# Kernel optimization log

Hardware: AMD Instinct MI355X
Metric: run time of the kernel (lower is better)

## Reference

```python
import jax, jax.numpy as jnp
import numpy as np

B, C, K = 128, 32, 128


def setup_inputs() -> dict:
    key = jax.random.key(0)
    k1, k2, k3, k4, k5 = jax.random.split(key, 5)
    x = jax.random.normal(k1, (B, 1, K, K), dtype=jnp.float32)
    # Conv2d(1, C, (1, K)) weight -> effectively [C, K] over the column axis
    w_col = jax.random.normal(k2, (C, K), dtype=jnp.float32) * (1.0 / np.sqrt(K))
    b_col = jax.random.normal(k3, (C,), dtype=jnp.float32) * 0.01
    # Conv2d(1, C, (K, 1)) weight -> effectively [C, K] over the row axis
    w_row = jax.random.normal(k4, (C, K), dtype=jnp.float32) * (1.0 / np.sqrt(K))
    b_row = jax.random.normal(k5, (C,), dtype=jnp.float32) * 0.01
    return {"x": x, "w_col": w_col, "b_col": b_col, "w_row": w_row, "b_row": b_row}


def reference(x, w_col, b_col, w_row, b_row):
    xs = x[:, 0]  # [B, K, K]
    # conv_column: kernel (1, K) contracts the column axis j -> [B, C, K] (rows i)
    col = jnp.einsum("bij,cj->bci", xs, w_col) + b_col[None, :, None]
    # conv_row: kernel (K, 1) contracts the row axis i -> [B, C, K] (cols j)
    row = jnp.einsum("bij,ci->bcj", xs, w_row) + b_row[None, :, None]
    # Tiling conv_row to [B,C,K,K] (identical rows) and conv_column to
    # [B,C,K,K] (identical columns) and matmul-ing yields, for every (i, j):
    #   out[b,c,i,j] = sum_k row[b,c,k] * col[b,c,k]
    # i.e. a per-(b,c) scalar broadcast over the K x K plane.
    s = jnp.einsum("bck,bck->bc", row, col)  # [B, C]
    return jnp.broadcast_to(s[:, :, None, None], (x.shape[0], w_col.shape[0], K, K))
```

## Files before the change

### kernel.cpp

```cpp
#include <hip/hip_runtime.h>
#include <hip/hip_bf16.h>


constexpr int KDIM = 128;
constexpr int CDIM = 32;
constexpr int LD   = 132;

__device__ __forceinline__ int swz_word(int row, int col) {
    return (row << 7) | ((((col >> 2) ^ ((row >> 2) & 7)) << 2) | (col & 3));
}

__global__ __launch_bounds__(512) void fused_kernel(
    const float* __restrict__ x,
    const float* __restrict__ w_col, const float* __restrict__ b_col,
    const float* __restrict__ w_row, const float* __restrict__ b_row,
    float* __restrict__ out)
{
    __shared__ float  xs[KDIM * LD];
    __shared__ float  xt[KDIM * KDIM];
    __shared__ float2 wpr[KDIM][8];
    __shared__ float2 wpc[KDIM][8];
    __shared__ float  s_lds[16];

    const int bid = blockIdx.x;
    const int xcd = bid & 7;
    const int idx = bid >> 3;
    const int b   = xcd * 16 + (idx >> 1);
    const int ch  = idx & 1;
    const int C0  = ch * 16;
    const int tid = threadIdx.x;

    #pragma unroll
    for (int e = 0; e < 2; ++e) {
        const int ent = tid + 512 * e;
        const int i   = ent & 127;
        const int g   = ent >> 7;
        wpr[i][g] = make_float2(w_row[(C0 + g) * KDIM + i],
                                w_row[(C0 + g + 8) * KDIM + i]);
        wpc[i][g] = make_float2(w_col[(C0 + g) * KDIM + i],
                                w_col[(C0 + g + 8) * KDIM + i]);
    }

    const float4* xsrc = reinterpret_cast<const float4*>(x + (size_t)b * KDIM * KDIM);
    const int tj  = tid & 31;
    const int ti0 = tid >> 5;
    #pragma unroll
    for (int it = 0; it < 2; ++it) {
        const int ti = ti0 + 16 * it;
        const float4 r0 = xsrc[(4 * ti + 0) * 32 + tj];
        const float4 r1 = xsrc[(4 * ti + 1) * 32 + tj];
        const float4 r2 = xsrc[(4 * ti + 2) * 32 + tj];
        const float4 r3 = xsrc[(4 * ti + 3) * 32 + tj];
        *reinterpret_cast<float4*>(&xs[(4 * ti + 0) * LD + 4 * tj]) = r0;
        *reinterpret_cast<float4*>(&xs[(4 * ti + 1) * LD + 4 * tj]) = r1;
        *reinterpret_cast<float4*>(&xs[(4 * ti + 2) * LD + 4 * tj]) = r2;
        *reinterpret_cast<float4*>(&xs[(4 * ti + 3) * LD + 4 * tj]) = r3;
        *reinterpret_cast<float4*>(&xt[swz_word(4 * tj + 0, 4 * ti)]) =
            make_float4(r0.x, r1.x, r2.x, r3.x);
        *reinterpret_cast<float4*>(&xt[swz_word(4 * tj + 1, 4 * ti)]) =
            make_float4(r0.y, r1.y, r2.y, r3.y);
        *reinterpret_cast<float4*>(&xt[swz_word(4 * tj + 2, 4 * ti)]) =
            make_float4(r0.z, r1.z, r2.z, r3.z);
        *reinterpret_cast<float4*>(&xt[swz_word(4 * tj + 3, 4 * ti)]) =
            make_float4(r0.w, r1.w, r2.w, r3.w);
    }
    __syncthreads();

    const int w    = tid >> 6;
    const int lane = tid & 63;
    const int kq   = lane & 31;
    const int ih   = lane >> 5;
    const int k0   = 4 * kq;

    float au0[4] = {0,0,0,0}, au1[4] = {0,0,0,0};
    float av0[4] = {0,0,0,0}, av1[4] = {0,0,0,0};

    #pragma unroll 4
    for (int ii = 0; ii < 64; ++ii) {
        const int i = ih * 64 + ii;
        const float4 xv = *reinterpret_cast<const float4*>(&xs[i * LD + k0]);
        const float4 tv = *reinterpret_cast<const float4*>(&xt[swz_word(i, k0)]);
        const float2 wu = wpr[i][w];
        const float2 wv = wpc[i][w];
        au0[0] = fmaf(wu.x, xv.x, au0[0]); au0[1] = fmaf(wu.x, xv.y, au0[1]);
        au0[2] = fmaf(wu.x, xv.z, au0[2]); au0[3] = fmaf(wu.x, xv.w, au0[3]);
        au1[0] = fmaf(wu.y, xv.x, au1[0]); au1[1] = fmaf(wu.y, xv.y, au1[1]);
        au1[2] = fmaf(wu.y, xv.z, au1[2]); au1[3] = fmaf(wu.y, xv.w, au1[3]);
        av0[0] = fmaf(wv.x, tv.x, av0[0]); av0[1] = fmaf(wv.x, tv.y, av0[1]);
        av0[2] = fmaf(wv.x, tv.z, av0[2]); av0[3] = fmaf(wv.x, tv.w, av0[3]);
        av1[0] = fmaf(wv.y, tv.x, av1[0]); av1[1] = fmaf(wv.y, tv.y, av1[1]);
        av1[2] = fmaf(wv.y, tv.z, av1[2]); av1[3] = fmaf(wv.y, tv.w, av1[3]);
    }

    #pragma unroll
    for (int q = 0; q < 4; ++q) {
        au0[q] += __shfl_xor(au0[q], 32);
        au1[q] += __shfl_xor(au1[q], 32);
        av0[q] += __shfl_xor(av0[q], 32);
        av1[q] += __shfl_xor(av1[q], 32);
    }
    const int c0 = C0 + w, c1 = C0 + w + 8;
    const float br0 = b_row[c0], bc0 = b_col[c0];
    const float br1 = b_row[c1], bc1 = b_col[c1];

    float p0 = 0.f, p1 = 0.f;
    #pragma unroll
    for (int q = 0; q < 4; ++q) {
        p0 += (au0[q] + br0) * (av0[q] + bc0);
        p1 += (au1[q] + br1) * (av1[q] + bc1);
    }
    #pragma unroll
    for (int off = 1; off < 32; off <<= 1) {
        p0 += __shfl_xor(p0, off);
        p1 += __shfl_xor(p1, off);
    }
    if (lane == 0) { s_lds[w] = p0; s_lds[w + 8] = p1; }
    __syncthreads();

    float4* out4 = reinterpret_cast<float4*>(out);
    #pragma unroll
    for (int cl = 0; cl < 16; ++cl) {
        const float val = s_lds[cl];
        float4 v4;
        v4.x = v4.y = v4.z = v4.w = val;
        float4* o = out4 + (size_t)(b * CDIM + C0 + cl) * 4096;
        #pragma unroll
        for (int r = 0; r < 8; ++r) {
            o[tid + 512 * r] = v4;
        }
    }
}

extern "C" void kernel_launch(void* const* d_in, const int* in_sizes, int n_in,
                              void* d_out, int out_size, void* d_ws, size_t ws_size,
                              hipStream_t stream) {
    const float* x     = (const float*)d_in[0];
    const float* w_col = (const float*)d_in[1];
    const float* b_col = (const float*)d_in[2];
    const float* w_row = (const float*)d_in[3];
    const float* b_row = (const float*)d_in[4];
    float* out = (float*)d_out;

    fused_kernel<<<256, 512, 0, stream>>>(x, w_col, b_col, w_row, b_row, out);
}
```

Baseline: 52.20 us.

## Pack x and its transpose as bf16 pairs in one LDS array; per-wave output stores

```diff
diff --git a/kernel.cpp b/kernel.cpp
--- a/kernel.cpp
+++ b/kernel.cpp
@@ -4,10 +4,13 @@
 
 constexpr int KDIM = 128;
 constexpr int CDIM = 32;
-constexpr int LD   = 132;
 
-__device__ __forceinline__ int swz_word(int row, int col) {
-    return (row << 7) | ((((col >> 2) ^ ((row >> 2) & 7)) << 2) | (col & 3));
+__device__ __forceinline__ uint32_t bf16rne(float f) {
+    const uint32_t u = __float_as_uint(f);
+    return (u + 0x7FFFu + ((u >> 16) & 1u)) >> 16;
+}
+__device__ __forceinline__ uint32_t pack2(float lo, float hi) {
+    return bf16rne(lo) | (bf16rne(hi) << 16);
 }
 
 __global__ __launch_bounds__(512) void fused_kernel(
@@ -16,29 +19,28 @@
     const float* __restrict__ w_row, const float* __restrict__ b_row,
     float* __restrict__ out)
 {
-    __shared__ float  xs[KDIM * LD];
-    __shared__ float  xt[KDIM * KDIM];
-    __shared__ float2 wpr[KDIM][8];
-    __shared__ float2 wpc[KDIM][8];
-    __shared__ float  s_lds[16];
+    __shared__ uint32_t xz[KDIM * KDIM];
+    __shared__ float4   wall[KDIM][8];
 
-    const int bid = blockIdx.x;
-    const int xcd = bid & 7;
-    const int idx = bid >> 3;
-    const int b   = xcd * 16 + (idx >> 1);
-    const int ch  = idx & 1;
-    const int C0  = ch * 16;
-    const int tid = threadIdx.x;
+    const int bid  = blockIdx.x;
+    const int xcd  = bid & 7;
+    const int idx  = bid >> 3;
+    const int b    = xcd * 16 + (idx >> 1);
+    const int ch   = idx & 1;
+    const int C0   = ch * 16;
+    const int tid  = threadIdx.x;
+    const int w    = tid >> 6;
+    const int lane = tid & 63;
 
     #pragma unroll
     for (int e = 0; e < 2; ++e) {
         const int ent = tid + 512 * e;
         const int i   = ent & 127;
         const int g   = ent >> 7;
-        wpr[i][g] = make_float2(w_row[(C0 + g) * KDIM + i],
-                                w_row[(C0 + g + 8) * KDIM + i]);
-        wpc[i][g] = make_float2(w_col[(C0 + g) * KDIM + i],
-                                w_col[(C0 + g + 8) * KDIM + i]);
+        wall[i][g] = make_float4(w_row[(C0 + g) * KDIM + i],
+                                 w_row[(C0 + g + 8) * KDIM + i],
+                                 w_col[(C0 + g) * KDIM + i],
+                                 w_col[(C0 + g + 8) * KDIM + i]);
     }
 
     const float4* xsrc = reinterpret_cast<const float4*>(x + (size_t)b * KDIM * KDIM);
@@ -47,49 +49,45 @@
     #pragma unroll
     for (int it = 0; it < 2; ++it) {
         const int ti = ti0 + 16 * it;
-        const float4 r0 = xsrc[(4 * ti + 0) * 32 + tj];
-        const float4 r1 = xsrc[(4 * ti + 1) * 32 + tj];
-        const float4 r2 = xsrc[(4 * ti + 2) * 32 + tj];
-        const float4 r3 = xsrc[(4 * ti + 3) * 32 + tj];
-        *reinterpret_cast<float4*>(&xs[(4 * ti + 0) * LD + 4 * tj]) = r0;
-        *reinterpret_cast<float4*>(&xs[(4 * ti + 1) * LD + 4 * tj]) = r1;
-        *reinterpret_cast<float4*>(&xs[(4 * ti + 2) * LD + 4 * tj]) = r2;
-        *reinterpret_cast<float4*>(&xs[(4 * ti + 3) * LD + 4 * tj]) = r3;
-        *reinterpret_cast<float4*>(&xt[swz_word(4 * tj + 0, 4 * ti)]) =
-            make_float4(r0.x, r1.x, r2.x, r3.x);
-        *reinterpret_cast<float4*>(&xt[swz_word(4 * tj + 1, 4 * ti)]) =
-            make_float4(r0.y, r1.y, r2.y, r3.y);
-        *reinterpret_cast<float4*>(&xt[swz_word(4 * tj + 2, 4 * ti)]) =
-            make_float4(r0.z, r1.z, r2.z, r3.z);
-        *reinterpret_cast<float4*>(&xt[swz_word(4 * tj + 3, 4 * ti)]) =
-            make_float4(r0.w, r1.w, r2.w, r3.w);
+        float4 A[4], Bq[4];
+        #pragma unroll
+        for (int r = 0; r < 4; ++r) A[r]  = xsrc[(4 * ti + r) * 32 + tj];
+        #pragma unroll
+        for (int r = 0; r < 4; ++r) Bq[r] = xsrc[(4 * tj + r) * 32 + ti];
+        #pragma unroll
+        for (int r = 0; r < 4; ++r) {
+            uint4 e;
+            e.x = pack2(A[r].x, (&Bq[0].x)[r]);
+            e.y = pack2(A[r].y, (&Bq[1].x)[r]);
+            e.z = pack2(A[r].z, (&Bq[2].x)[r]);
+            e.w = pack2(A[r].w, (&Bq[3].x)[r]);
+            *reinterpret_cast<uint4*>(&xz[(4 * ti + r) * KDIM + 4 * tj]) = e;
+        }
     }
     __syncthreads();
 
-    const int w    = tid >> 6;
-    const int lane = tid & 63;
-    const int kq   = lane & 31;
-    const int ih   = lane >> 5;
-    const int k0   = 4 * kq;
+    const int kq = lane & 31;
+    const int ih = lane >> 5;
+    const int k0 = 4 * kq;
 
     float au0[4] = {0,0,0,0}, au1[4] = {0,0,0,0};
     float av0[4] = {0,0,0,0}, av1[4] = {0,0,0,0};
 
-    #pragma unroll 4
+    #pragma unroll 8
     for (int ii = 0; ii < 64; ++ii) {
         const int i = ih * 64 + ii;
-        const float4 xv = *reinterpret_cast<const float4*>(&xs[i * LD + k0]);
-        const float4 tv = *reinterpret_cast<const float4*>(&xt[swz_word(i, k0)]);
-        const float2 wu = wpr[i][w];
-        const float2 wv = wpc[i][w];
-        au0[0] = fmaf(wu.x, xv.x, au0[0]); au0[1] = fmaf(wu.x, xv.y, au0[1]);
-        au0[2] = fmaf(wu.x, xv.z, au0[2]); au0[3] = fmaf(wu.x, xv.w, au0[3]);
-        au1[0] = fmaf(wu.y, xv.x, au1[0]); au1[1] = fmaf(wu.y, xv.y, au1[1]);
-        au1[2] = fmaf(wu.y, xv.z, au1[2]); au1[3] = fmaf(wu.y, xv.w, au1[3]);
-        av0[0] = fmaf(wv.x, tv.x, av0[0]); av0[1] = fmaf(wv.x, tv.y, av0[1]);
-        av0[2] = fmaf(wv.x, tv.z, av0[2]); av0[3] = fmaf(wv.x, tv.w, av0[3]);
-        av1[0] = fmaf(wv.y, tv.x, av1[0]); av1[1] = fmaf(wv.y, tv.y, av1[1]);
-        av1[2] = fmaf(wv.y, tv.z, av1[2]); av1[3] = fmaf(wv.y, tv.w, av1[3]);
+        const uint4  z  = *reinterpret_cast<const uint4*>(&xz[i * KDIM + k0]);
+        const float4 wq = wall[i][w];
+        const uint32_t zz[4] = {z.x, z.y, z.z, z.w};
+        #pragma unroll
+        for (int q = 0; q < 4; ++q) {
+            const float xlo = __uint_as_float(zz[q] << 16);
+            const float xhi = __uint_as_float(zz[q] & 0xFFFF0000u);
+            au0[q] = fmaf(wq.x, xlo, au0[q]);
+            au1[q] = fmaf(wq.y, xlo, au1[q]);
+            av0[q] = fmaf(wq.z, xhi, av0[q]);
+            av1[q] = fmaf(wq.w, xhi, av1[q]);
+        }
     }
 
     #pragma unroll
@@ -114,21 +112,15 @@
         p0 += __shfl_xor(p0, off);
         p1 += __shfl_xor(p1, off);
     }
-    if (lane == 0) { s_lds[w] = p0; s_lds[w + 8] = p1; }
-    __syncthreads();
 
-    float4* out4 = reinterpret_cast<float4*>(out);
+    float4 v0; v0.x = v0.y = v0.z = v0.w = p0;
+    float4 v1; v1.x = v1.y = v1.z = v1.w = p1;
+    float4* o0 = reinterpret_cast<float4*>(out) + (size_t)(b * CDIM + c0) * 4096;
+    float4* o1 = reinterpret_cast<float4*>(out) + (size_t)(b * CDIM + c1) * 4096;
     #pragma unroll
-    for (int cl = 0; cl < 16; ++cl) {
-        const float val = s_lds[cl];
-        float4 v4;
-        v4.x = v4.y = v4.z = v4.w = val;
-        float4* o = out4 + (size_t)(b * CDIM + C0 + cl) * 4096;
-        #pragma unroll
-        for (int r = 0; r < 8; ++r) {
-            o[tid + 512 * r] = v4;
-        }
-    }
+    for (int r = 0; r < 64; ++r) o0[lane + 64 * r] = v0;
+    #pragma unroll
+    for (int r = 0; r < 64; ++r) o1[lane + 64 * r] = v1;
 }
 
 extern "C" void kernel_launch(void* const* d_in, const int* in_sizes, int n_in,
```

Result: slower. 54.52 us (+4.4%).

## Split waves into row/column roles computing four channels each from LDS

Applied to the files above, without the earlier changes.

```diff
diff --git a/kernel.cpp b/kernel.cpp
--- a/kernel.cpp
+++ b/kernel.cpp
@@ -4,7 +4,6 @@
 
 constexpr int KDIM = 128;
 constexpr int CDIM = 32;
-constexpr int LD   = 132;
 
 __device__ __forceinline__ int swz_word(int row, int col) {
     return (row << 7) | ((((col >> 2) ^ ((row >> 2) & 7)) << 2) | (col & 3));
@@ -16,29 +15,32 @@
     const float* __restrict__ w_row, const float* __restrict__ b_row,
     float* __restrict__ out)
 {
-    __shared__ float  xs[KDIM * LD];
-    __shared__ float  xt[KDIM * KDIM];
-    __shared__ float2 wpr[KDIM][8];
-    __shared__ float2 wpc[KDIM][8];
-    __shared__ float  s_lds[16];
+    __shared__ __align__(16) float xs[KDIM * KDIM];
+    __shared__ __align__(16) float xt[KDIM * KDIM];
+    __shared__ float4 wu4[KDIM][4];
+    __shared__ float4 wc4[KDIM][4];
 
-    const int bid = blockIdx.x;
-    const int xcd = bid & 7;
-    const int idx = bid >> 3;
-    const int b   = xcd * 16 + (idx >> 1);
-    const int ch  = idx & 1;
-    const int C0  = ch * 16;
-    const int tid = threadIdx.x;
+    const int bid  = blockIdx.x;
+    const int xcd  = bid & 7;
+    const int idx  = bid >> 3;
+    const int b    = xcd * 16 + (idx >> 1);
+    const int ch   = idx & 1;
+    const int C0   = ch * 16;
+    const int tid  = threadIdx.x;
+    const int w    = tid >> 6;
+    const int lane = tid & 63;
 
-    #pragma unroll
-    for (int e = 0; e < 2; ++e) {
-        const int ent = tid + 512 * e;
-        const int i   = ent & 127;
-        const int g   = ent >> 7;
-        wpr[i][g] = make_float2(w_row[(C0 + g) * KDIM + i],
-                                w_row[(C0 + g + 8) * KDIM + i]);
-        wpc[i][g] = make_float2(w_col[(C0 + g) * KDIM + i],
-                                w_col[(C0 + g + 8) * KDIM + i]);
+    {
+        const int i = tid & 127;
+        const int g = tid >> 7;
+        wu4[i][g] = make_float4(w_row[(C0 + 4 * g + 0) * KDIM + i],
+                                w_row[(C0 + 4 * g + 1) * KDIM + i],
+                                w_row[(C0 + 4 * g + 2) * KDIM + i],
+                                w_row[(C0 + 4 * g + 3) * KDIM + i]);
+        wc4[i][g] = make_float4(w_col[(C0 + 4 * g + 0) * KDIM + i],
+                                w_col[(C0 + 4 * g + 1) * KDIM + i],
+                                w_col[(C0 + 4 * g + 2) * KDIM + i],
+                                w_col[(C0 + 4 * g + 3) * KDIM + i]);
     }
 
     const float4* xsrc = reinterpret_cast<const float4*>(x + (size_t)b * KDIM * KDIM);
@@ -51,10 +53,10 @@
         const float4 r1 = xsrc[(4 * ti + 1) * 32 + tj];
         const float4 r2 = xsrc[(4 * ti + 2) * 32 + tj];
         const float4 r3 = xsrc[(4 * ti + 3) * 32 + tj];
-        *reinterpret_cast<float4*>(&xs[(4 * ti + 0) * LD + 4 * tj]) = r0;
-        *reinterpret_cast<float4*>(&xs[(4 * ti + 1) * LD + 4 * tj]) = r1;
-        *reinterpret_cast<float4*>(&xs[(4 * ti + 2) * LD + 4 * tj]) = r2;
-        *reinterpret_cast<float4*>(&xs[(4 * ti + 3) * LD + 4 * tj]) = r3;
+        *reinterpret_cast<float4*>(&xs[(4 * ti + 0) * KDIM + 4 * tj]) = r0;
+        *reinterpret_cast<float4*>(&xs[(4 * ti + 1) * KDIM + 4 * tj]) = r1;
+        *reinterpret_cast<float4*>(&xs[(4 * ti + 2) * KDIM + 4 * tj]) = r2;
+        *reinterpret_cast<float4*>(&xs[(4 * ti + 3) * KDIM + 4 * tj]) = r3;
         *reinterpret_cast<float4*>(&xt[swz_word(4 * tj + 0, 4 * ti)]) =
             make_float4(r0.x, r1.x, r2.x, r3.x);
         *reinterpret_cast<float4*>(&xt[swz_word(4 * tj + 1, 4 * ti)]) =
@@ -66,61 +68,84 @@
     }
     __syncthreads();
 
-    const int w    = tid >> 6;
-    const int lane = tid & 63;
+    const int role = w >> 2;
+    const int g    = w & 3;
     const int kq   = lane & 31;
     const int ih   = lane >> 5;
     const int k0   = 4 * kq;
 
-    float au0[4] = {0,0,0,0}, au1[4] = {0,0,0,0};
-    float av0[4] = {0,0,0,0}, av1[4] = {0,0,0,0};
+    float a[4][4] = {{0,0,0,0},{0,0,0,0},{0,0,0,0},{0,0,0,0}};
 
-    #pragma unroll 4
-    for (int ii = 0; ii < 64; ++ii) {
-        const int i = ih * 64 + ii;
-        const float4 xv = *reinterpret_cast<const float4*>(&xs[i * LD + k0]);
-        const float4 tv = *reinterpret_cast<const float4*>(&xt[swz_word(i, k0)]);
-        const float2 wu = wpr[i][w];
-        const float2 wv = wpc[i][w];
-        au0[0] = fmaf(wu.x, xv.x, au0[0]); au0[1] = fmaf(wu.x, xv.y, au0[1]);
-        au0[2] = fmaf(wu.x, xv.z, au0[2]); au0[3] = fmaf(wu.x, xv.w, au0[3]);
-        au1[0] = fmaf(wu.y, xv.x, au1[0]); au1[1] = fmaf(wu.y, xv.y, au1[1]);
-        au1[2] = fmaf(wu.y, xv.z, au1[2]); au1[3] = fmaf(wu.y, xv.w, au1[3]);
-        av0[0] = fmaf(wv.x, tv.x, av0[0]); av0[1] = fmaf(wv.x, tv.y, av0[1]);
-        av0[2] = fmaf(wv.x, tv.z, av0[2]); av0[3] = fmaf(wv.x, tv.w, av0[3]);
-        av1[0] = fmaf(wv.y, tv.x, av1[0]); av1[1] = fmaf(wv.y, tv.y, av1[1]);
-        av1[2] = fmaf(wv.y, tv.z, av1[2]); av1[3] = fmaf(wv.y, tv.w, av1[3]);
+    if (role == 0) {
+        #pragma unroll 8
+        for (int ii = 0; ii < 64; ++ii) {
+            const int i = ih * 64 + ii;
+            const float4 xv = *reinterpret_cast<const float4*>(&xs[i * KDIM + k0]);
+            const float4 wq = wu4[i][g];
+            #pragma unroll
+            for (int cc = 0; cc < 4; ++cc) {
+                const float ww = (&wq.x)[cc];
+                a[cc][0] = fmaf(ww, xv.x, a[cc][0]);
+                a[cc][1] = fmaf(ww, xv.y, a[cc][1]);
+                a[cc][2] = fmaf(ww, xv.z, a[cc][2]);
+                a[cc][3] = fmaf(ww, xv.w, a[cc][3]);
+            }
+        }
+    } else {
+        #pragma unroll 8
+        for (int ii = 0; ii < 64; ++ii) {
+            const int j = ih * 64 + ii;
+            const float4 tv = *reinterpret_cast<const float4*>(&xt[swz_word(j, k0)]);
+            const float4 wq = wc4[j][g];
+            #pragma unroll
+            for (int cc = 0; cc < 4; ++cc) {
+                const float ww = (&wq.x)[cc];
+                a[cc][0] = fmaf(ww, tv.x, a[cc][0]);
+                a[cc][1] = fmaf(ww, tv.y, a[cc][1]);
+                a[cc][2] = fmaf(ww, tv.z, a[cc][2]);
+                a[cc][3] = fmaf(ww, tv.w, a[cc][3]);
+            }
+        }
     }
 
     #pragma unroll
-    for (int q = 0; q < 4; ++q) {
-        au0[q] += __shfl_xor(au0[q], 32);
-        au1[q] += __shfl_xor(au1[q], 32);
-        av0[q] += __shfl_xor(av0[q], 32);
-        av1[q] += __shfl_xor(av1[q], 32);
+    for (int cc = 0; cc < 4; ++cc)
+        #pragma unroll
+        for (int q = 0; q < 4; ++q)
+            a[cc][q] += __shfl_xor(a[cc][q], 32);
+
+    __syncthreads();
+
+    if (lane < 32) {
+        float* ex = xs + role * 2048;
+        #pragma unroll
+        for (int cc = 0; cc < 4; ++cc) {
+            *reinterpret_cast<float4*>(&ex[(4 * g + cc) * KDIM + k0]) =
+                make_float4(a[cc][0], a[cc][1], a[cc][2], a[cc][3]);
+        }
     }
-    const int c0 = C0 + w, c1 = C0 + w + 8;
-    const float br0 = b_row[c0], bc0 = b_col[c0];
-    const float br1 = b_row[c1], bc1 = b_col[c1];
+    __syncthreads();
 
-    float p0 = 0.f, p1 = 0.f;
-    #pragma unroll
-    for (int q = 0; q < 4; ++q) {
-        p0 += (au0[q] + br0) * (av0[q] + bc0);
-        p1 += (au1[q] + br1) * (av1[q] + bc1);
+    {
+        const int cg  = tid >> 5;
+        const int kq2 = tid & 31;
+        const float4 uu = *reinterpret_cast<const float4*>(&xs[cg * KDIM + 4 * kq2]);
+        const float4 vv = *reinterpret_cast<const float4*>(&xs[2048 + cg * KDIM + 4 * kq2]);
+        const int c = C0 + cg;
+        const float br = b_row[c];
+        const float bc = b_col[c];
+        float p = (uu.x + br) * (vv.x + bc) + (uu.y + br) * (vv.y + bc)
+                + (uu.z + br) * (vv.z + bc) + (uu.w + br) * (vv.w + bc);
+        #pragma unroll
+        for (int off = 1; off < 32; off <<= 1) p += __shfl_xor(p, off, 32);
+        if (kq2 == 0) xt[cg] = p;
     }
-    #pragma unroll
-    for (int off = 1; off < 32; off <<= 1) {
-        p0 += __shfl_xor(p0, off);
-        p1 += __shfl_xor(p1, off);
-    }
-    if (lane == 0) { s_lds[w] = p0; s_lds[w + 8] = p1; }
     __syncthreads();
 
     float4* out4 = reinterpret_cast<float4*>(out);
     #pragma unroll
     for (int cl = 0; cl < 16; ++cl) {
-        const float val = s_lds[cl];
+        const float val = xt[cl];
         float4 v4;
         v4.x = v4.y = v4.z = v4.w = val;
         float4* o = out4 + (size_t)(b * CDIM + C0 + cl) * 4096;
```

New measurement: 52.03 us. No clear change (-0.3%).
